# Kernel tuning notes

Hardware: AMD Instinct MI355X
Metric: run time of the kernel (lower is better)

## Reference

```python
import jax, jax.numpy as jnp
import numpy as np

HARD_ANGLE = 15.0  # degrees, from PMLoss __init__ default
NUM_CLASSES = 22
NUM_POINTS = 2048
BATCH = 32


def quat_to_rotmat(q):
    # q: [..., 4] in (w, x, y, z) order (PoseCNN convention); assumes unit norm
    w, x, y, z = q[..., 0], q[..., 1], q[..., 2], q[..., 3]
    R = jnp.stack([
        1 - 2 * (y * y + z * z), 2 * (x * y - z * w), 2 * (x * z + y * w),
        2 * (x * y + z * w), 1 - 2 * (x * x + z * z), 2 * (y * z - x * w),
        2 * (x * z - y * w), 2 * (y * z + x * w), 1 - 2 * (x * x + y * y)],
        axis=-1)
    return R.reshape(q.shape[:-1] + (3, 3))


def smooth_l1(x):
    ax = jnp.abs(x)
    return jnp.where(ax < 1.0, 0.5 * x * x, ax - 0.5)


def setup_inputs() -> dict:
    key = jax.random.key(0)
    k1, k2, k3, k4 = jax.random.split(key, 4)
    B, C, P = BATCH, NUM_CLASSES, NUM_POINTS
    # unit quaternions per (sample, class)
    q_pred = jax.random.normal(k1, (B, C, 4), dtype=jnp.float32)
    q_pred = q_pred / jnp.linalg.norm(q_pred, axis=-1, keepdims=True)
    q_gt = jax.random.normal(k2, (B, C, 4), dtype=jnp.float32)
    q_gt = q_gt / jnp.linalg.norm(q_gt, axis=-1, keepdims=True)
    prediction = q_pred.reshape(B, 4 * C)
    target = q_gt.reshape(B, 4 * C)
    # one active class per sample: weight block of ones at that class
    cls = jax.random.randint(k3, (B,), 1, C)  # skip background class 0
    weight = jnp.zeros((B, C, 4), dtype=jnp.float32)
    weight = weight.at[jnp.arange(B), cls, :].set(1.0).reshape(B, 4 * C)
    # model point clouds, roughly object-scale (~10 cm)
    points = 0.1 * jax.random.normal(k4, (C, P, 3), dtype=jnp.float32)
    # half the classes symmetric
    symmetry = (jnp.arange(C) % 2).astype(jnp.float32)
    return {"prediction": prediction, "target": target, "weight": weight,
            "points": points, "symmetry": symmetry}


def reference(prediction, target, weight, points, symmetry):
    B = prediction.shape[0]
    C = symmetry.shape[0]
    P = points.shape[1]
    # class per sample = first class with weight > 0 (CUDA scans stride-4 w slot)
    wsel = weight.reshape(B, C, 4)[:, :, 0]           # [B, C]
    cls = jnp.argmax(wsel > 0, axis=1)                # [B]
    valid = (jnp.max(wsel, axis=1) > 0)               # [B] samples with a class
    bidx = jnp.arange(B)
    q_pred = prediction.reshape(B, C, 4)[bidx, cls]   # [B, 4]
    q_gt = target.reshape(B, C, 4)[bidx, cls]         # [B, 4]
    R_pred = quat_to_rotmat(q_pred)                   # [B, 3, 3]
    R_gt = quat_to_rotmat(q_gt)
    pts = points[cls]                                 # [B, P, 3]
    p_pred = jnp.einsum('bij,bpj->bpi', R_pred, pts)  # [B, P, 3]
    p_gt = jnp.einsum('bij,bpj->bpi', R_gt, pts)      # [B, P, 3]
    # angular distance between quaternions, in degrees
    dot = jnp.abs(jnp.sum(q_pred * q_gt, axis=1))
    ang = 2.0 * jnp.arccos(jnp.clip(dot, 0.0, 1.0)) * (180.0 / jnp.pi)
    use_closest = (symmetry[cls] > 0) & (ang > HARD_ANGLE)  # [B]
    # pairwise squared distances without materializing [B,P,P,3]
    d2 = (jnp.sum(p_pred * p_pred, axis=-1)[:, :, None]
          + jnp.sum(p_gt * p_gt, axis=-1)[:, None, :]
          - 2.0 * jnp.einsum('bpi,bqi->bpq', p_pred, p_gt))  # [B, P, P]
    nn_idx = jnp.argmin(d2, axis=-1)                         # [B, P]
    p_gt_nn = jnp.take_along_axis(p_gt, nn_idx[..., None], axis=1)
    matched = jnp.where(use_closest[:, None, None], p_gt_nn, p_gt)
    diff = p_pred - matched                                   # [B, P, 3]
    per_sample = jnp.sum(smooth_l1(diff), axis=(1, 2)) * valid.astype(diff.dtype)
    loss = jnp.sum(per_sample) / jnp.asarray(B * P, dtype=diff.dtype)
    return loss
```

## Files before the change

kernel.cpp:

```cpp
#include <hip/hip_runtime.h>

#define NPTS 2048
#define QC 32
#define G  (NPTS / QC)
#define RP 8
#define HARD_COS 0.9914448613738104f
#define META_FLOATS 24
#define PRED_OFF 1024

__global__ void pm_prep(const float* __restrict__ pred,
                        const float* __restrict__ tgt,
                        const float* __restrict__ wgt,
                        const float* __restrict__ sym,
                        float* __restrict__ ws,
                        float* __restrict__ out,
                        int B, int C) {
    int b = blockIdx.x * blockDim.x + threadIdx.x;
    if (b == 0) out[0] = 0.0f;
    if (b >= B) return;

    int cls = 0; float valid = 0.0f;
    for (int c = 0; c < C; ++c) {
        if (wgt[b * 4 * C + c * 4] > 0.0f) { cls = c; valid = 1.0f; break; }
    }
    const float* qp = pred + b * 4 * C + cls * 4;
    const float* qg = tgt  + b * 4 * C + cls * 4;
    float pw = qp[0], px = qp[1], py = qp[2], pz = qp[3];
    float gw = qg[0], gx = qg[1], gy = qg[2], gz = qg[3];

    float* o = ws + (size_t)b * META_FLOATS;
    o[0] = 1.f - 2.f * (py * py + pz * pz);
    o[1] = 2.f * (px * py - pz * pw);
    o[2] = 2.f * (px * pz + py * pw);
    o[3] = 2.f * (px * py + pz * pw);
    o[4] = 1.f - 2.f * (px * px + pz * pz);
    o[5] = 2.f * (py * pz - px * pw);
    o[6] = 2.f * (px * pz - py * pw);
    o[7] = 2.f * (py * pz + px * pw);
    o[8] = 1.f - 2.f * (px * px + py * py);
    o[9]  = 1.f - 2.f * (gy * gy + gz * gz);
    o[10] = 2.f * (gx * gy - gz * gw);
    o[11] = 2.f * (gx * gz + gy * gw);
    o[12] = 2.f * (gx * gy + gz * gw);
    o[13] = 1.f - 2.f * (gx * gx + gz * gz);
    o[14] = 2.f * (gy * gz - gx * gw);
    o[15] = 2.f * (gx * gz - gy * gw);
    o[16] = 2.f * (gy * gz + gx * gw);
    o[17] = 1.f - 2.f * (gx * gx + gy * gy);

    float dot = fabsf(pw * gw + px * gx + py * gy + pz * gz);
    dot = fminf(fmaxf(dot, 0.0f), 1.0f);
    float uc = (sym[cls] > 0.0f && dot < HARD_COS) ? 1.0f : 0.0f;
    o[18] = (float)cls;
    o[19] = valid;
    o[20] = uc;
}

__global__ __launch_bounds__(256) void pm_rotate(const float* __restrict__ points,
                                                 float* __restrict__ ws,
                                                 int gt_off) {
    const int b = blockIdx.y;
    const int side = blockIdx.x;
    const float* o = ws + (size_t)b * META_FLOATS;
    if (o[19] == 0.0f) return;
    const int mbase = (side == 0) ? 0 : 9;
    const float m0 = o[mbase + 0], m1 = o[mbase + 1], m2 = o[mbase + 2],
                m3 = o[mbase + 3], m4 = o[mbase + 4], m5 = o[mbase + 5],
                m6 = o[mbase + 6], m7 = o[mbase + 7], m8 = o[mbase + 8];
    const int cls = (int)o[18];
    const float* pts = points + (size_t)cls * NPTS * 3;
    float4* dst = (float4*)(ws + (side == 0 ? PRED_OFF : gt_off)) + (size_t)b * NPTS;
    const int tid = threadIdx.x;
#pragma unroll
    for (int r = 0; r < RP; ++r) {
        int i = r * 256 + tid;
        float x = pts[i * 3 + 0], y = pts[i * 3 + 1], z = pts[i * 3 + 2];
        float ax = m0 * x + m1 * y + m2 * z;
        float ay = m3 * x + m4 * y + m5 * z;
        float az = m6 * x + m7 * y + m8 * z;
        float w = (side == 0) ? 0.0f : (ax * ax + ay * ay + az * az);
        dst[i] = make_float4(ax, ay, az, w);
    }
}

__global__ __launch_bounds__(256) void pm_partial(float* __restrict__ ws,
                                                  int gt_off, int cand_off) {
    const int b  = blockIdx.y;
    const int qc = blockIdx.x;
    const float* o = ws + (size_t)b * META_FLOATS;
    if (o[19] == 0.0f || o[20] == 0.0f) return;

    const float4* pred_rot = (const float4*)(ws + PRED_OFF) + (size_t)b * NPTS;
    const float4* gt_rot   = (const float4*)(ws + gt_off)   + (size_t)b * NPTS;
    const int tid = threadIdx.x;

    __shared__ float4 gt[G];
    if (tid < G) gt[tid] = gt_rot[qc * G + tid];
    __syncthreads();

    float nx[RP], ny[RP], nz[RP], bd[RP];
    int bi[RP];
#pragma unroll
    for (int r = 0; r < RP; ++r) {
        float4 pp = pred_rot[r * 256 + tid];
        nx[r] = -2.0f * pp.x; ny[r] = -2.0f * pp.y; nz[r] = -2.0f * pp.z;
        bd[r] = 3.4e38f; bi[r] = 0;
    }

#pragma unroll 4
    for (int j = 0; j < G; ++j) {
        float4 g = gt[j];
#pragma unroll
        for (int r = 0; r < RP; ++r) {
            float d = __fmaf_rn(nx[r], g.x,
                      __fmaf_rn(ny[r], g.y,
                      __fmaf_rn(nz[r], g.z, g.w)));
            if (d < bd[r]) { bd[r] = d; bi[r] = j; }
        }
    }

    float* cand = ws + cand_off + ((size_t)b * QC + qc) * NPTS;
#pragma unroll
    for (int r = 0; r < RP; ++r) {
        int p = r * 256 + tid;
        cand[p] = (float)(qc * G + bi[r]);
    }
}

__device__ __forceinline__ float smooth_l1(float x) {
    float ax = fabsf(x);
    return (ax < 1.0f) ? 0.5f * x * x : ax - 0.5f;
}

__global__ __launch_bounds__(256) void pm_final(float* __restrict__ ws,
                                                float* __restrict__ out,
                                                int gt_off, int cand_off,
                                                float inv_bp) {
    __shared__ float partial[4];
    const int b = blockIdx.y;
    const float* o = ws + (size_t)b * META_FLOATS;
    const int tid = threadIdx.x;
    float acc = 0.0f;

    if (o[19] != 0.0f) {
        const float4* pred_rot = (const float4*)(ws + PRED_OFF) + (size_t)b * NPTS;
        const float4* gt_rot   = (const float4*)(ws + gt_off)   + (size_t)b * NPTS;
        const int p = blockIdx.x * 256 + tid;
        float4 pp = pred_rot[p];
        float mx, my, mz;
        if (o[20] != 0.0f) {
            const float nx = -2.0f * pp.x, ny = -2.0f * pp.y, nz = -2.0f * pp.z;
            const float* cand = ws + cand_off + (size_t)b * QC * NPTS + p;
            float bd = 3.4e38f; int bq = 0;
#pragma unroll 8
            for (int qc = 0; qc < QC; ++qc) {
                int q = (int)cand[(size_t)qc * NPTS];
                float4 g = gt_rot[q];
                float d = __fmaf_rn(nx, g.x,
                          __fmaf_rn(ny, g.y,
                          __fmaf_rn(nz, g.z, g.w)));
                if (d < bd) { bd = d; bq = q; }
            }
            float4 g = gt_rot[bq];
            mx = g.x; my = g.y; mz = g.z;
        } else {
            float4 g = gt_rot[p];
            mx = g.x; my = g.y; mz = g.z;
        }
        acc = smooth_l1(pp.x - mx) + smooth_l1(pp.y - my) + smooth_l1(pp.z - mz);
    }

    for (int off = 32; off > 0; off >>= 1) acc += __shfl_down(acc, off);
    if ((tid & 63) == 0) partial[tid >> 6] = acc;
    __syncthreads();
    if (tid == 0) {
        float s = partial[0] + partial[1] + partial[2] + partial[3];
        atomicAdd(out, s * inv_bp);
    }
}

extern "C" void kernel_launch(void* const* d_in, const int* in_sizes, int n_in,
                              void* d_out, int out_size, void* d_ws, size_t ws_size,
                              hipStream_t stream) {
    const float* pred = (const float*)d_in[0];
    const float* tgt  = (const float*)d_in[1];
    const float* wgt  = (const float*)d_in[2];
    const float* pts  = (const float*)d_in[3];
    const float* sym  = (const float*)d_in[4];
    float* out = (float*)d_out;
    float* ws  = (float*)d_ws;

    const int C = in_sizes[4];
    const int B = in_sizes[0] / (4 * C);

    const int gt_off   = PRED_OFF + B * NPTS * 4;
    const int cand_off = gt_off   + B * NPTS * 4;

    pm_prep<<<1, 64, 0, stream>>>(pred, tgt, wgt, sym, ws, out, B, C);
    dim3 gridR(2, B);
    pm_rotate<<<gridR, 256, 0, stream>>>(pts, ws, gt_off);
    dim3 gridP(QC, B);
    pm_partial<<<gridP, 256, 0, stream>>>(ws, gt_off, cand_off);
    dim3 gridF(NPTS / 256, B);
    pm_final<<<gridF, 256, 0, stream>>>(ws, out, gt_off, cand_off,
                                        1.0f / (float)(B * NPTS));
}
```

Measured before the change: 95.23 us.

## Fuse prep into rotate kernel and store candidate distances to skip regather

Merges the per-sample quaternion setup into the point-rotation kernel, removing one launch and the metadata round trip. The partial nearest-neighbour kernel now stores each chunk's best distance alongside its index. The final kernel can then pick the minimum directly instead of gathering and recomputing 32 candidate distances. This doubles the size of the candidate buffer written and read, and each thread of the setup kernel redundantly scans the weights for the class.

After: 107.1 us. 1.12x slower.

```diff
diff --git a/kernel.cpp b/kernel.cpp
--- a/kernel.cpp
+++ b/kernel.cpp
@@ -5,81 +5,63 @@
 #define G  (NPTS / QC)
 #define RP 8
 #define HARD_COS 0.9914448613738104f
-#define META_FLOATS 24
+#define META_FLOATS 8
 #define PRED_OFF 1024
 
-__global__ void pm_prep(const float* __restrict__ pred,
-                        const float* __restrict__ tgt,
-                        const float* __restrict__ wgt,
-                        const float* __restrict__ sym,
-                        float* __restrict__ ws,
-                        float* __restrict__ out,
-                        int B, int C) {
-    int b = blockIdx.x * blockDim.x + threadIdx.x;
-    if (b == 0) out[0] = 0.0f;
-    if (b >= B) return;
+
+__global__ __launch_bounds__(256) void pm_setup(const float* __restrict__ pred,
+                                                const float* __restrict__ tgt,
+                                                const float* __restrict__ wgt,
+                                                const float* __restrict__ sym,
+                                                const float* __restrict__ points,
+                                                float* __restrict__ ws,
+                                                float* __restrict__ out,
+                                                int B, int C, int gt_off) {
+    const int b = blockIdx.y;
+    const int side = blockIdx.x;
 
     int cls = 0; float valid = 0.0f;
     for (int c = 0; c < C; ++c) {
         if (wgt[b * 4 * C + c * 4] > 0.0f) { cls = c; valid = 1.0f; break; }
     }
-    const float* qp = pred + b * 4 * C + cls * 4;
-    const float* qg = tgt  + b * 4 * C + cls * 4;
-    float pw = qp[0], px = qp[1], py = qp[2], pz = qp[3];
-    float gw = qg[0], gx = qg[1], gy = qg[2], gz = qg[3];
 
-    float* o = ws + (size_t)b * META_FLOATS;
-    o[0] = 1.f - 2.f * (py * py + pz * pz);
-    o[1] = 2.f * (px * py - pz * pw);
-    o[2] = 2.f * (px * pz + py * pw);
-    o[3] = 2.f * (px * py + pz * pw);
-    o[4] = 1.f - 2.f * (px * px + pz * pz);
-    o[5] = 2.f * (py * pz - px * pw);
-    o[6] = 2.f * (px * pz - py * pw);
-    o[7] = 2.f * (py * pz + px * pw);
-    o[8] = 1.f - 2.f * (px * px + py * py);
-    o[9]  = 1.f - 2.f * (gy * gy + gz * gz);
-    o[10] = 2.f * (gx * gy - gz * gw);
-    o[11] = 2.f * (gx * gz + gy * gw);
-    o[12] = 2.f * (gx * gy + gz * gw);
-    o[13] = 1.f - 2.f * (gx * gx + gz * gz);
-    o[14] = 2.f * (gy * gz - gx * gw);
-    o[15] = 2.f * (gx * gz - gy * gw);
-    o[16] = 2.f * (gy * gz + gx * gw);
-    o[17] = 1.f - 2.f * (gx * gx + gy * gy);
+    const float* q = (side == 0 ? pred : tgt) + b * 4 * C + cls * 4;
+    const float w = q[0], x = q[1], y = q[2], z = q[3];
+    const float m0 = 1.f - 2.f * (y * y + z * z);
+    const float m1 = 2.f * (x * y - z * w);
+    const float m2 = 2.f * (x * z + y * w);
+    const float m3 = 2.f * (x * y + z * w);
+    const float m4 = 1.f - 2.f * (x * x + z * z);
+    const float m5 = 2.f * (y * z - x * w);
+    const float m6 = 2.f * (x * z - y * w);
+    const float m7 = 2.f * (y * z + x * w);
+    const float m8 = 1.f - 2.f * (x * x + y * y);
 
-    float dot = fabsf(pw * gw + px * gx + py * gy + pz * gz);
-    dot = fminf(fmaxf(dot, 0.0f), 1.0f);
-    float uc = (sym[cls] > 0.0f && dot < HARD_COS) ? 1.0f : 0.0f;
-    o[18] = (float)cls;
-    o[19] = valid;
-    o[20] = uc;
-}
-
-__global__ __launch_bounds__(256) void pm_rotate(const float* __restrict__ points,
-                                                 float* __restrict__ ws,
-                                                 int gt_off) {
-    const int b = blockIdx.y;
-    const int side = blockIdx.x;
-    const float* o = ws + (size_t)b * META_FLOATS;
-    if (o[19] == 0.0f) return;
-    const int mbase = (side == 0) ? 0 : 9;
-    const float m0 = o[mbase + 0], m1 = o[mbase + 1], m2 = o[mbase + 2],
-                m3 = o[mbase + 3], m4 = o[mbase + 4], m5 = o[mbase + 5],
-                m6 = o[mbase + 6], m7 = o[mbase + 7], m8 = o[mbase + 8];
-    const int cls = (int)o[18];
     const float* pts = points + (size_t)cls * NPTS * 3;
     float4* dst = (float4*)(ws + (side == 0 ? PRED_OFF : gt_off)) + (size_t)b * NPTS;
     const int tid = threadIdx.x;
+    if (valid != 0.0f) {
 #pragma unroll
-    for (int r = 0; r < RP; ++r) {
-        int i = r * 256 + tid;
-        float x = pts[i * 3 + 0], y = pts[i * 3 + 1], z = pts[i * 3 + 2];
-        float ax = m0 * x + m1 * y + m2 * z;
-        float ay = m3 * x + m4 * y + m5 * z;
-        float az = m6 * x + m7 * y + m8 * z;
-        float w = (side == 0) ? 0.0f : (ax * ax + ay * ay + az * az);
-        dst[i] = make_float4(ax, ay, az, w);
+        for (int r = 0; r < RP; ++r) {
+            int i = r * 256 + tid;
+            float px = pts[i * 3 + 0], py = pts[i * 3 + 1], pz = pts[i * 3 + 2];
+            float ax = m0 * px + m1 * py + m2 * pz;
+            float ay = m3 * px + m4 * py + m5 * pz;
+            float az = m6 * px + m7 * py + m8 * pz;
+            float ww = (side == 0) ? 0.0f : (ax * ax + ay * ay + az * az);
+            dst[i] = make_float4(ax, ay, az, ww);
+        }
+    }
+
+    if (side == 0 && tid == 0) {
+        const float* qp = pred + b * 4 * C + cls * 4;
+        const float* qg = tgt  + b * 4 * C + cls * 4;
+        float dot = fabsf(qp[0] * qg[0] + qp[1] * qg[1] + qp[2] * qg[2] + qp[3] * qg[3]);
+        dot = fminf(fmaxf(dot, 0.0f), 1.0f);
+        float uc = (sym[cls] > 0.0f && dot < HARD_COS) ? 1.0f : 0.0f;
+        ws[b * META_FLOATS + 0] = valid;
+        ws[b * META_FLOATS + 1] = uc;
+        if (b == 0) out[0] = 0.0f;
     }
 }
 
@@ -87,8 +69,7 @@
                                                   int gt_off, int cand_off) {
     const int b  = blockIdx.y;
     const int qc = blockIdx.x;
-    const float* o = ws + (size_t)b * META_FLOATS;
-    if (o[19] == 0.0f || o[20] == 0.0f) return;
+    if (ws[b * META_FLOATS + 0] == 0.0f || ws[b * META_FLOATS + 1] == 0.0f) return;
 
     const float4* pred_rot = (const float4*)(ws + PRED_OFF) + (size_t)b * NPTS;
     const float4* gt_rot   = (const float4*)(ws + gt_off)   + (size_t)b * NPTS;
@@ -119,11 +100,11 @@
         }
     }
 
-    float* cand = ws + cand_off + ((size_t)b * QC + qc) * NPTS;
+    float2* cand = (float2*)(ws + cand_off) + ((size_t)b * QC + qc) * NPTS;
 #pragma unroll
     for (int r = 0; r < RP; ++r) {
         int p = r * 256 + tid;
-        cand[p] = (float)(qc * G + bi[r]);
+        cand[p] = make_float2(bd[r], (float)(qc * G + bi[r]));
     }
 }
 
@@ -138,36 +119,28 @@
                                                 float inv_bp) {
     __shared__ float partial[4];
     const int b = blockIdx.y;
-    const float* o = ws + (size_t)b * META_FLOATS;
     const int tid = threadIdx.x;
     float acc = 0.0f;
 
-    if (o[19] != 0.0f) {
+    if (ws[b * META_FLOATS + 0] != 0.0f) {
         const float4* pred_rot = (const float4*)(ws + PRED_OFF) + (size_t)b * NPTS;
         const float4* gt_rot   = (const float4*)(ws + gt_off)   + (size_t)b * NPTS;
         const int p = blockIdx.x * 256 + tid;
         float4 pp = pred_rot[p];
-        float mx, my, mz;
-        if (o[20] != 0.0f) {
-            const float nx = -2.0f * pp.x, ny = -2.0f * pp.y, nz = -2.0f * pp.z;
-            const float* cand = ws + cand_off + (size_t)b * QC * NPTS + p;
+        float4 g;
+        if (ws[b * META_FLOATS + 1] != 0.0f) {
+            const float2* cand = (const float2*)(ws + cand_off) + (size_t)b * QC * NPTS + p;
             float bd = 3.4e38f; int bq = 0;
-#pragma unroll 8
+#pragma unroll
             for (int qc = 0; qc < QC; ++qc) {
-                int q = (int)cand[(size_t)qc * NPTS];
-                float4 g = gt_rot[q];
-                float d = __fmaf_rn(nx, g.x,
-                          __fmaf_rn(ny, g.y,
-                          __fmaf_rn(nz, g.z, g.w)));
-                if (d < bd) { bd = d; bq = q; }
+                float2 cq = cand[(size_t)qc * NPTS];
+                if (cq.x < bd) { bd = cq.x; bq = (int)cq.y; }
             }
-            float4 g = gt_rot[bq];
-            mx = g.x; my = g.y; mz = g.z;
+            g = gt_rot[bq];
         } else {
-            float4 g = gt_rot[p];
-            mx = g.x; my = g.y; mz = g.z;
+            g = gt_rot[p];
         }
-        acc = smooth_l1(pp.x - mx) + smooth_l1(pp.y - my) + smooth_l1(pp.z - mz);
+        acc = smooth_l1(pp.x - g.x) + smooth_l1(pp.y - g.y) + smooth_l1(pp.z - g.z);
     }
 
     for (int off = 32; off > 0; off >>= 1) acc += __shfl_down(acc, off);
@@ -196,9 +169,8 @@
     const int gt_off   = PRED_OFF + B * NPTS * 4;
     const int cand_off = gt_off   + B * NPTS * 4;
 
-    pm_prep<<<1, 64, 0, stream>>>(pred, tgt, wgt, sym, ws, out, B, C);
-    dim3 gridR(2, B);
-    pm_rotate<<<gridR, 256, 0, stream>>>(pts, ws, gt_off);
+    dim3 gridS(2, B);
+    pm_setup<<<gridS, 256, 0, stream>>>(pred, tgt, wgt, sym, pts, ws, out, B, C, gt_off);
     dim3 gridP(QC, B);
     pm_partial<<<gridP, 256, 0, stream>>>(ws, gt_off, cand_off);
     dim3 gridF(NPTS / 256, B);
```
